# Performance work log

Measured on AMD Instinct MI355X. Metric: run time of the kernel, lower is better.

## Reference

```python
import jax, jax.numpy as jnp
import numpy as np

D_MODEL = 1024
N_HEADS = 16
HEAD_DIM = D_MODEL // N_HEADS
HIDDEN = 4096
EPS = 1e-5


def setup_inputs() -> dict:
    key = jax.random.key(0)
    ks = jax.random.split(key, 16)
    s = 1.0 / np.sqrt(D_MODEL)
    sh = 1.0 / np.sqrt(HIDDEN)
    inp = {
        'x': jax.random.normal(ks[0], (4, 2048, D_MODEL), dtype=jnp.float32),
        'Wq': jax.random.normal(ks[1], (D_MODEL, D_MODEL), dtype=jnp.float32) * s,
        'bq': jnp.zeros((D_MODEL,), jnp.float32),
        'Wk': jax.random.normal(ks[2], (D_MODEL, D_MODEL), dtype=jnp.float32) * s,
        'bk': jnp.zeros((D_MODEL,), jnp.float32),
        'Wv': jax.random.normal(ks[3], (D_MODEL, D_MODEL), dtype=jnp.float32) * s,
        'bv': jnp.zeros((D_MODEL,), jnp.float32),
        'Wo': jax.random.normal(ks[4], (D_MODEL, D_MODEL), dtype=jnp.float32) * s,
        'bo': jnp.zeros((D_MODEL,), jnp.float32),
        'gamma1': jnp.ones((D_MODEL,), jnp.float32),
        'beta1': jnp.zeros((D_MODEL,), jnp.float32),
        'W1': jax.random.normal(ks[5], (D_MODEL, HIDDEN), dtype=jnp.float32) * s,
        'b1': jnp.zeros((HIDDEN,), jnp.float32),
        'W2': jax.random.normal(ks[6], (HIDDEN, D_MODEL), dtype=jnp.float32) * sh,
        'b2': jnp.zeros((D_MODEL,), jnp.float32),
        'gamma2': jnp.ones((D_MODEL,), jnp.float32),
        'beta2': jnp.zeros((D_MODEL,), jnp.float32),
    }
    return inp


def _layernorm(x, gamma, beta):
    mu = jnp.mean(x, axis=-1, keepdims=True)
    var = jnp.mean(jnp.square(x - mu), axis=-1, keepdims=True)
    return (x - mu) * jax.lax.rsqrt(var + EPS) * gamma + beta


def _encoder_layer(x, Wq, bq, Wk, bk, Wv, bv, Wo, bo, gamma1, beta1,
                   W1, b1, W2, b2, gamma2, beta2):
    B, S, _ = x.shape
    # projections -> [B, H, S, Dh]
    def split_heads(t):
        return t.reshape(B, S, N_HEADS, HEAD_DIM).transpose(0, 2, 1, 3)
    q = split_heads(x @ Wq + bq)
    k = split_heads(x @ Wk + bk)
    v = split_heads(x @ Wv + bv)
    scale = 1.0 / jnp.sqrt(jnp.float32(HEAD_DIM))
    scores = jnp.einsum('bhqd,bhkd->bhqk', q, k) * scale
    attn = jax.nn.softmax(scores, axis=-1)
    ctx = jnp.einsum('bhqk,bhkd->bhqd', attn, v)
    ctx = ctx.transpose(0, 2, 1, 3).reshape(B, S, D_MODEL)
    attn_out = ctx @ Wo + bo
    # post-norm residual 1
    h = _layernorm(x + attn_out, gamma1, beta1)
    # MLP with exact (erf) GELU, as torch F.gelu default
    mlp = jax.nn.gelu(h @ W1 + b1, approximate=False) @ W2 + b2
    return _layernorm(h + mlp, gamma2, beta2)


def reference(x, Wq, bq, Wk, bk, Wv, bv, Wo, bo, gamma1, beta1,
              W1, b1, W2, b2, gamma2, beta2):
    return _encoder_layer(x, Wq, bq, Wk, bk, Wv, bv, Wo, bo, gamma1, beta1,
                          W1, b1, W2, b2, gamma2, beta2)
```

## Files before the change

kernel.cpp:

```cpp
#include <hip/hip_runtime.h>
#include <cstdint>
#include <cstddef>

using u16 = unsigned short;
using bf16x8 = __attribute__((ext_vector_type(8))) short;
using f32x4  = __attribute__((ext_vector_type(4))) float;

__device__ __forceinline__ u16 f2bf(float f) {
    union { float f; unsigned u; } v; v.f = f;
    unsigned r = v.u + 0x7fffu + ((v.u >> 16) & 1u);
    return (u16)(r >> 16);
}

__device__ __forceinline__ float bf2f(u16 b) {
    union { unsigned u; float f; } v; v.u = (unsigned)b << 16;
    return v.f;
}

__device__ __forceinline__ unsigned cvtpk(float lo, float hi) {
    unsigned r;
    asm("v_cvt_pk_bf16_f32 %0, %1, %2" : "=v"(r) : "v"(lo), "v"(hi));
    return r;
}

__device__ __forceinline__ float fexp2(float x) {
    float r;
    asm("v_exp_f32 %0, %1" : "=v"(r) : "v"(x));
    return r;
}

__device__ __forceinline__ float gelu_f(float x) {
    const float t2 = fminf(x * fmaf(0.10294825f, x * x, 2.3022082f), 80.f);
    const float e  = fexp2(t2);
    return x * e * __frcp_rn(e + 1.0f);
}

__device__ __forceinline__ void gld_lds16(const void* g, void* l) {
    __builtin_amdgcn_global_load_lds(
        (__attribute__((address_space(1))) void*)g,
        (__attribute__((address_space(3))) void*)l, 16, 0, 0);
}

__device__ __forceinline__ f32x4 mfma16(bf16x8 a, bf16x8 b, f32x4 c) {
    return __builtin_amdgcn_mfma_f32_16x16x32_bf16(a, b, c, 0, 0, 0);
}

__global__ __launch_bounds__(256)
void cast_kernel(const float* __restrict__ in, u16* __restrict__ out, int n8) {
    int i = blockIdx.x * 256 + threadIdx.x;
    if (i >= n8) return;
    const float4* p = (const float4*)in;
    float4 a = p[i * 2], b = p[i * 2 + 1];
    ushort4 r0 = make_ushort4(f2bf(a.x), f2bf(a.y), f2bf(a.z), f2bf(a.w));
    ushort4 r1 = make_ushort4(f2bf(b.x), f2bf(b.y), f2bf(b.z), f2bf(b.w));
    ((ushort4*)out)[i * 2]     = r0;
    ((ushort4*)out)[i * 2 + 1] = r1;
}

__global__ __launch_bounds__(256)
void tcast_all_kernel(const float* __restrict__ Wq, const float* __restrict__ Wk,
                      const float* __restrict__ Wv, const float* __restrict__ Wo,
                      const float* __restrict__ W1, const float* __restrict__ W2,
                      u16* __restrict__ wqkvt, u16* __restrict__ wot,
                      u16* __restrict__ w1t, u16* __restrict__ w2t)
{
    const int g = blockIdx.x;
    const float* src; u16* dst; int K, N, ti; float scale = 1.0f;
    if (g < 1024)      { src = Wq; dst = wqkvt;               K = 1024; N = 1024; ti = g;        scale = 0.18033688011112042f; }
    else if (g < 2048) { src = Wk; dst = wqkvt + 1048576;     K = 1024; N = 1024; ti = g - 1024; }
    else if (g < 3072) { src = Wv; dst = wqkvt + 2097152;     K = 1024; N = 1024; ti = g - 2048; }
    else if (g < 4096) { src = Wo; dst = wot;                 K = 1024; N = 1024; ti = g - 3072; }
    else if (g < 8192) { src = W1; dst = w1t;                 K = 1024; N = 4096; ti = g - 4096; }
    else               { src = W2; dst = w2t;                 K = 4096; N = 1024; ti = g - 8192; }
    const int nt = N >> 5;
    const int bx = ti % nt, by = ti / nt;
    const int k0 = by * 32, n0 = bx * 32;

    __shared__ float tile[32][33];
    const int tx = threadIdx.x & 31, ty = threadIdx.x >> 5;
    #pragma unroll
    for (int r = 0; r < 4; ++r) {
        int k = ty * 4 + r;
        tile[k][tx] = src[(size_t)(k0 + k) * N + n0 + tx];
    }
    __syncthreads();
    #pragma unroll
    for (int r = 0; r < 4; ++r) {
        int n = ty * 4 + r;
        dst[(size_t)(n0 + n) * K + k0 + tx] = f2bf(tile[tx][n] * scale);
    }
}

__global__ __launch_bounds__(256)
void bias_concat_kernel(const float* __restrict__ bq, const float* __restrict__ bk,
                        const float* __restrict__ bv, float* __restrict__ out) {
    int i = blockIdx.x * 256 + threadIdx.x;
    if (i >= 3072) return;
    float v;
    if (i < 1024)      v = bq[i] * 0.18033688011112042f;
    else if (i < 2048) v = bk[i - 1024];
    else               v = bv[i - 2048];
    out[i] = v;
}

template <int BM, int EPI>
__global__ __launch_bounds__(512, 1)
void gemm_pipe_kernel(const u16* __restrict__ A, const u16* __restrict__ Bt,
                      const float* __restrict__ bias, void* __restrict__ Cout,
                      int M, int N, int K)
{
    constexpr int AH  = BM * 64;
    constexpr int BH  = 16384;
    constexpr int BUF = 2 * AH + 2 * BH;
    constexpr int LPA = BM / 128;
    constexpr int VMN = LPA + 2;
    constexpr int MR  = BM / 32;
    constexpr int MRH = MR / 2;

    extern __shared__ char smem[];

    const int tid  = threadIdx.x;
    const int wid  = tid >> 6, lane = tid & 63;
    const int l15  = lane & 15, l4 = lane >> 4;
    const int wm   = wid >> 2, wn = wid & 3;

    const int nwg = gridDim.x;
    const int qx = nwg >> 3, rx = nwg & 7;
    const int orig = blockIdx.x;
    const int xcd = orig & 7, jx = orig >> 3;
    const int wgid = (xcd < rx ? xcd * (qx + 1) : rx * (qx + 1) + (xcd - rx) * qx) + jx;
    const int NTn = N / 256;
    const int m0 = (wgid / NTn) * BM;
    const int n0 = (wgid % NTn) * 256;

    const int q0 = tid >> 3, g0 = tid & 7;
    const int u0 = g0 ^ (q0 & 7);
    const int r0 = (q0 << 1) | (u0 >> 2), c80 = u0 & 3;
    const int q1 = q0 + 64;
    const int u1 = g0 ^ (q1 & 7);
    const int r1 = (q1 << 1) | (u1 >> 2), c81 = u1 & 3;
    const u16* aP0 = A  + (size_t)(m0 + r0) * K + c80 * 8;
    const u16* aP1 = A  + (size_t)(m0 + r1) * K + c81 * 8;
    const u16* bP0 = Bt + (size_t)(n0 + r0) * K + c80 * 8;
    const u16* bP1 = Bt + (size_t)(n0 + r1) * K + c81 * 8;
    const int NT = K >> 6;

    auto stageA = [&](int tt, int kk, int nb) {
        char* dst = smem + nb * BUF + kk * AH + tid * 16;
        const int kte = (tt << 6) + (kk << 5);
        gld_lds16(aP0 + kte, dst);
        if constexpr (LPA == 2) gld_lds16(aP1 + kte, dst + 8192);
    };
    auto stageB = [&](int tt, int kk, int nb) {
        char* dst = smem + nb * BUF + 2 * AH + kk * BH + tid * 16;
        const int kte = (tt << 6) + (kk << 5);
        gld_lds16(bP0 + kte, dst);
        gld_lds16(bP1 + kte, dst + 8192);
    };

    auto frag_off = [&](int row) -> int {
        const int q = row >> 1;
        const int u = ((row & 1) << 2) | l4;
        const int g = u ^ (q & 7);
        return q * 128 + g * 16;
    };

    f32x4 acc[MR][4];
    #pragma unroll
    for (int i = 0; i < MR; ++i)
        #pragma unroll
        for (int jj = 0; jj < 4; ++jj) acc[i][jj] = f32x4{0.f, 0.f, 0.f, 0.f};

    stageA(0, 0, 0); stageB(0, 0, 0); stageA(0, 1, 0); stageB(0, 1, 0);
    if constexpr (VMN == 4) asm volatile("s_waitcnt vmcnt(4)" ::: "memory");
    else                    asm volatile("s_waitcnt vmcnt(3)" ::: "memory");
    __builtin_amdgcn_s_barrier();
    asm volatile("" ::: "memory");

    for (int t = 0; t < NT; ++t) {
        const int cur = t & 1, nb = cur ^ 1;
        const int tn = (t + 1 < NT) ? t + 1 : t;
        const char* buf = smem + cur * BUF;
        bf16x8 bfr[4], af[MRH];

        #pragma unroll
        for (int kk = 0; kk < 2; ++kk) {
            #pragma unroll
            for (int fc = 0; fc < 4; ++fc)
                bfr[fc] = *(const bf16x8*)(buf + 2 * AH + kk * BH +
                                           frag_off(wn * 64 + fc * 16 + l15));
            #pragma unroll
            for (int i = 0; i < MRH; ++i)
                af[i] = *(const bf16x8*)(buf + kk * AH +
                                         frag_off(wm * (BM / 2) + i * 16 + l15));
            stageA(tn, kk, nb);
            asm volatile("" ::: "memory");
            __builtin_amdgcn_s_barrier();
            asm volatile("" ::: "memory");
            __builtin_amdgcn_s_setprio(1);
            #pragma unroll
            for (int i = 0; i < MRH; ++i)
                #pragma unroll
                for (int fc = 0; fc < 4; ++fc)
                    acc[i][fc] = mfma16(af[i], bfr[fc], acc[i][fc]);
            __builtin_amdgcn_s_setprio(0);

            #pragma unroll
            for (int i = 0; i < MRH; ++i)
                af[i] = *(const bf16x8*)(buf + kk * AH +
                                         frag_off(wm * (BM / 2) + (MRH + i) * 16 + l15));
            stageB(tn, kk, nb);
            if constexpr (VMN == 4) asm volatile("s_waitcnt vmcnt(4)" ::: "memory");
            else                    asm volatile("s_waitcnt vmcnt(3)" ::: "memory");
            __builtin_amdgcn_s_barrier();
            asm volatile("" ::: "memory");
            __builtin_amdgcn_s_setprio(1);
            #pragma unroll
            for (int i = 0; i < MRH; ++i)
                #pragma unroll
                for (int fc = 0; fc < 4; ++fc)
                    acc[MRH + i][fc] = mfma16(af[i], bfr[fc], acc[MRH + i][fc]);
            __builtin_amdgcn_s_setprio(0);
            asm volatile("" ::: "memory");
        }
    }

    float bv[4];
    #pragma unroll
    for (int fc = 0; fc < 4; ++fc) bv[fc] = bias[n0 + wn * 64 + fc * 16 + l15];
    #pragma unroll
    for (int fr = 0; fr < MR; ++fr) {
        const int rowg = m0 + wm * (BM / 2) + fr * 16 + l4 * 4;
        #pragma unroll
        for (int fc = 0; fc < 4; ++fc) {
            const int colg = n0 + wn * 64 + fc * 16 + l15;
            #pragma unroll
            for (int r = 0; r < 4; ++r) {
                const float v = acc[fr][fc][r] + bv[fc];
                const size_t off = (size_t)(rowg + r) * N + colg;
                if (EPI == 0) ((u16*)Cout)[off] = f2bf(v);
                else          ((u16*)Cout)[off] = f2bf(gelu_f(v));
            }
        }
    }
}

__global__ __launch_bounds__(256)
void vtrans_kernel(const u16* __restrict__ QKV, u16* __restrict__ Vt) {
    __shared__ u16 tile[64][68];
    const int t  = threadIdx.x;
    const int st = blockIdx.x, bh = blockIdx.y;
    const int b  = bh >> 4, h = bh & 15;
    #pragma unroll
    for (int i = 0; i < 2; ++i) {
        int sl = i * 32 + (t >> 3);
        const u16* gp = QKV + ((size_t)b * 2048 + st * 64 + sl) * 3072 + 2048 + h * 64 + (t & 7) * 8;
        ushort4 a = *(const ushort4*)gp;
        ushort4 c = *(const ushort4*)(gp + 4);
        u16* lp = &tile[sl][(t & 7) * 8];
        *(ushort4*)lp       = a;
        *(ushort4*)(lp + 4) = c;
    }
    __syncthreads();
    #pragma unroll
    for (int i = 0; i < 2; ++i) {
        int d  = i * 32 + (t >> 3);
        int s8 = (t & 7) * 8;
        ushort4 o0, o1;
        o0.x = tile[s8 + 0][d]; o0.y = tile[s8 + 1][d]; o0.z = tile[s8 + 2][d]; o0.w = tile[s8 + 3][d];
        o1.x = tile[s8 + 4][d]; o1.y = tile[s8 + 5][d]; o1.z = tile[s8 + 6][d]; o1.w = tile[s8 + 7][d];
        u16* op = Vt + ((size_t)bh * 64 + d) * 2048 + st * 64 + s8;
        *(ushort4*)op       = o0;
        *(ushort4*)(op + 4) = o1;
    }
}

__global__ __launch_bounds__(512)
void attn_kernel(const u16* __restrict__ QKV, const u16* __restrict__ Vt,
                 u16* __restrict__ ctx)
{
    __shared__ u16 smem[24576];

    const int tid = threadIdx.x;
    const int wid = tid >> 6, lane = tid & 63;
    const int l15 = lane & 15, l4 = lane >> 4;
    const int sw  = l15 & 7;
    const int lr  = lane >> 3;
    const int gsrc = ((lane & 7) ^ lr) * 8;
    const int g   = blockIdx.x;
    const int bh  = (g & 7) | ((g >> 6) << 3);
    const int qt  = (g >> 3) & 7;
    const int b = bh >> 4, h = bh & 15;
    const size_t qrow0 = (size_t)b * 2048 + (size_t)qt * 256;

    u16* const K0 = smem + 16384;
    u16* const V0 = smem + 20480;
    u16* const K1 = smem;
    u16* const V1 = smem + 4096;

    const u16* Qbase = QKV + h * 64;
    const u16* Kbase = QKV + (size_t)b * 2048 * 3072 + 1024 + h * 64;
    const u16* Vbase = Vt + (size_t)bh * 64 * 2048;

    #pragma unroll
    for (int c = 0; c < 4; ++c) {
        const int chunk = wid * 4 + c;
        const int row = chunk * 8 + lr;
        gld_lds16(Qbase + (qrow0 + row) * 3072 + gsrc,
                  (char*)smem + chunk * 1024);
    }

    auto stage_kv = [&](int kt, u16* kb, u16* vb) {
        const int rho = wid * 8 + lr;
        const int krow = (rho & 32) + ((rho & 16) >> 2) + ((rho & 12) << 1) + (rho & 3);
        gld_lds16(Kbase + (size_t)(kt + krow) * 3072 + gsrc,
                  (char*)kb + wid * 1024);
        gld_lds16(Vbase + (size_t)rho * 2048 + kt + gsrc,
                  (char*)vb + wid * 1024);
    };

    stage_kv(0, K0, V0);
    __syncthreads();

    bf16x8 qf[2][2];
    #pragma unroll
    for (int mi = 0; mi < 2; ++mi)
        #pragma unroll
        for (int kk = 0; kk < 2; ++kk)
            qf[mi][kk] = *(const bf16x8*)
                &smem[(size_t)(wid * 32 + mi * 16 + l15) * 64 + (((kk * 4 + l4) ^ sw) * 8)];
    __syncthreads();

    f32x4 accO[2][4] = {};
    f32x4 accL[2] = {};
    const short one_bf = (short)0x3F80;
    const bf16x8 ones = {one_bf, one_bf, one_bf, one_bf,
                         one_bf, one_bf, one_bf, one_bf};

    union U4 { unsigned u[4]; bf16x8 v; };

    auto compute_tile = [&](const u16* kb, const u16* vb) {
        f32x4 st[2][4];
        #pragma unroll
        for (int mi = 0; mi < 2; ++mi)
            #pragma unroll
            for (int ni = 0; ni < 4; ++ni) st[mi][ni] = f32x4{0.f, 0.f, 0.f, 0.f};
        __builtin_amdgcn_s_setprio(1);
        #pragma unroll
        for (int ni = 0; ni < 4; ++ni) {
            bf16x8 kf0 = *(const bf16x8*)&kb[(ni * 16 + l15) * 64 + ((l4 ^ sw) * 8)];
            bf16x8 kf1 = *(const bf16x8*)&kb[(ni * 16 + l15) * 64 + (((4 + l4) ^ sw) * 8)];
            #pragma unroll
            for (int mi = 0; mi < 2; ++mi) {
                st[mi][ni] = mfma16(kf0, qf[mi][0], st[mi][ni]);
                st[mi][ni] = mfma16(kf1, qf[mi][1], st[mi][ni]);
            }
        }
        __builtin_amdgcn_s_setprio(0);

        U4 pb[2][2];
        #pragma unroll
        for (int mi = 0; mi < 2; ++mi) {
            float p[4][4];
            #pragma unroll
            for (int ni = 0; ni < 4; ++ni)
                #pragma unroll
                for (int r = 0; r < 4; ++r)
                    p[ni][r] = fexp2(st[mi][ni][r]);
            #pragma unroll
            for (int ni = 0; ni < 4; ++ni) {
                pb[mi][ni >> 1].u[(ni & 1) * 2 + 0] = cvtpk(p[ni][0], p[ni][1]);
                pb[mi][ni >> 1].u[(ni & 1) * 2 + 1] = cvtpk(p[ni][2], p[ni][3]);
            }
        }

        __builtin_amdgcn_s_setprio(1);
        #pragma unroll
        for (int mi = 0; mi < 2; ++mi) {
            accL[mi] = mfma16(ones, pb[mi][0].v, accL[mi]);
            accL[mi] = mfma16(ones, pb[mi][1].v, accL[mi]);
        }
        #pragma unroll
        for (int di = 0; di < 4; ++di) {
            bf16x8 vf0 = *(const bf16x8*)&vb[(di * 16 + l15) * 64 + ((l4 ^ sw) * 8)];
            bf16x8 vf1 = *(const bf16x8*)&vb[(di * 16 + l15) * 64 + (((4 + l4) ^ sw) * 8)];
            #pragma unroll
            for (int mi = 0; mi < 2; ++mi) {
                accO[mi][di] = mfma16(vf0, pb[mi][0].v, accO[mi][di]);
                accO[mi][di] = mfma16(vf1, pb[mi][1].v, accO[mi][di]);
            }
        }
        __builtin_amdgcn_s_setprio(0);
    };

    for (int it = 0; it < 32; it += 2) {
        if (it + 1 < 32) stage_kv((it + 1) * 64, K1, V1);
        compute_tile(K0, V0);
        __syncthreads();
        if (it + 2 < 32) stage_kv((it + 2) * 64, K0, V0);
        compute_tile(K1, V1);
        __syncthreads();
    }

    #pragma unroll
    for (int mi = 0; mi < 2; ++mi) {
        const float inv = 1.0f / accL[mi][0];
        const size_t q = qrow0 + wid * 32 + mi * 16 + l15;
        #pragma unroll
        for (int di = 0; di < 4; ++di) {
            uint2 w;
            w.x = cvtpk(accO[mi][di][0] * inv, accO[mi][di][1] * inv);
            w.y = cvtpk(accO[mi][di][2] * inv, accO[mi][di][3] * inv);
            *(uint2*)&ctx[q * 1024 + h * 64 + di * 16 + l4 * 4] = w;
        }
    }
}

__global__ __launch_bounds__(256)
void add_ln_kernel(const u16* __restrict__ X, const u16* __restrict__ Y,
                   const float* __restrict__ gamma, const float* __restrict__ beta,
                   float* __restrict__ outf, u16* __restrict__ outb)
{
    const int row = blockIdx.x;
    const int t = threadIdx.x;
    const ushort4 xb = ((const ushort4*)(X + (size_t)row * 1024))[t];
    const ushort4 yb = ((const ushort4*)(Y + (size_t)row * 1024))[t];
    const float v0 = bf2f(xb.x) + bf2f(yb.x);
    const float v1 = bf2f(xb.y) + bf2f(yb.y);
    const float v2 = bf2f(xb.z) + bf2f(yb.z);
    const float v3 = bf2f(xb.w) + bf2f(yb.w);
    float s  = v0 + v1 + v2 + v3;
    float ss = v0 * v0 + v1 * v1 + v2 * v2 + v3 * v3;
    #pragma unroll
    for (int m = 1; m < 64; m <<= 1) {
        s  += __shfl_xor(s, m, 64);
        ss += __shfl_xor(ss, m, 64);
    }
    __shared__ float red[8];
    const int wid = t >> 6, lane = t & 63;
    if (lane == 0) { red[wid] = s; red[4 + wid] = ss; }
    __syncthreads();
    s  = red[0] + red[1] + red[2] + red[3];
    ss = red[4] + red[5] + red[6] + red[7];
    const float mu  = s * (1.f / 1024.f);
    const float var = ss * (1.f / 1024.f) - mu * mu;
    const float inv = rsqrtf(var + 1e-5f);
    const float4 g  = ((const float4*)gamma)[t];
    const float4 bb = ((const float4*)beta)[t];
    float4 o;
    o.x = (v0 - mu) * inv * g.x + bb.x;
    o.y = (v1 - mu) * inv * g.y + bb.y;
    o.z = (v2 - mu) * inv * g.z + bb.z;
    o.w = (v3 - mu) * inv * g.w + bb.w;
    if (outf != nullptr)
        ((float4*)(outf + (size_t)row * 1024))[t] = o;
    if (outb != nullptr) {
        ushort4 ob = make_ushort4(f2bf(o.x), f2bf(o.y), f2bf(o.z), f2bf(o.w));
        ((ushort4*)(outb + (size_t)row * 1024))[t] = ob;
    }
}

extern "C" void kernel_launch(void* const* d_in, const int* in_sizes, int n_in,
                              void* d_out, int out_size, void* d_ws, size_t ws_size,
                              hipStream_t stream)
{
    (void)in_sizes; (void)n_in; (void)out_size; (void)ws_size;
    const float* x   = (const float*)d_in[0];
    const float* Wq  = (const float*)d_in[1];
    const float* bq  = (const float*)d_in[2];
    const float* Wk  = (const float*)d_in[3];
    const float* bk  = (const float*)d_in[4];
    const float* Wv  = (const float*)d_in[5];
    const float* bv  = (const float*)d_in[6];
    const float* Wo  = (const float*)d_in[7];
    const float* bo  = (const float*)d_in[8];
    const float* g1  = (const float*)d_in[9];
    const float* be1 = (const float*)d_in[10];
    const float* W1  = (const float*)d_in[11];
    const float* b1  = (const float*)d_in[12];
    const float* W2  = (const float*)d_in[13];
    const float* b2  = (const float*)d_in[14];
    const float* g2  = (const float*)d_in[15];
    const float* be2 = (const float*)d_in[16];

    constexpr int M = 8192;
    constexpr int D = 1024;
    constexpr int F = 4096;

    char* ws = (char*)d_ws;
    size_t off = 0;
    auto nxt = [&](size_t bytes) -> char* {
        char* p = ws + off;
        off += (bytes + 255) & ~(size_t)255;
        return p;
    };
    u16*   xb    = (u16*)nxt((size_t)M * D * 2);
    u16*   wqkvt = (u16*)nxt((size_t)3 * D * D * 2);
    u16*   wot   = (u16*)nxt((size_t)D * D * 2);
    u16*   w1t   = (u16*)nxt((size_t)F * D * 2);
    u16*   w2t   = (u16*)nxt((size_t)D * F * 2);
    float* bqkv  = (float*)nxt(3072 * 4);
    u16*   qkv   = (u16*)nxt((size_t)M * 3 * D * 2);
    u16*   Vtb   = (u16*)nxt((size_t)M * D * 2);
    u16*   ctx   = (u16*)nxt((size_t)M * D * 2);
    u16*   attn  = (u16*)nxt((size_t)M * D * 2);
    u16*   hb    = (u16*)nxt((size_t)M * D * 2);
    u16*   t1    = qkv;
    u16*   mlp   = attn;

    cast_kernel<<<dim3(M * D / 8 / 256), dim3(256), 0, stream>>>(x, xb, M * D / 8);
    tcast_all_kernel<<<dim3(12288), dim3(256), 0, stream>>>(
        Wq, Wk, Wv, Wo, W1, W2, wqkvt, wot, w1t, w2t);
    bias_concat_kernel<<<dim3(12), dim3(256), 0, stream>>>(bq, bk, bv, bqkv);

    constexpr size_t LDS128 = 2 * (2 * 128 * 64 + 2 * 16384);
    constexpr size_t LDS256 = 2 * (2 * 256 * 64 + 2 * 16384);

    gemm_pipe_kernel<128, 0><<<dim3((M / 128) * (3 * D / 256)), dim3(512), LDS128, stream>>>(
        xb, wqkvt, bqkv, qkv, M, 3 * D, D);

    vtrans_kernel<<<dim3(2048 / 64, 64), dim3(256), 0, stream>>>(qkv, Vtb);
    attn_kernel<<<dim3(512), dim3(512), 0, stream>>>(qkv, Vtb, ctx);

    gemm_pipe_kernel<128, 0><<<dim3((M / 128) * (D / 256)), dim3(512), LDS128, stream>>>(
        ctx, wot, bo, attn, M, D, D);
    add_ln_kernel<<<dim3(M), dim3(256), 0, stream>>>(xb, attn, g1, be1, nullptr, hb);

    gemm_pipe_kernel<256, 2><<<dim3((M / 256) * (F / 256)), dim3(512), LDS256, stream>>>(
        hb, w1t, b1, t1, M, F, D);
    gemm_pipe_kernel<128, 0><<<dim3((M / 128) * (D / 256)), dim3(512), LDS128, stream>>>(
        t1, w2t, b2, mlp, M, D, F);
    add_ln_kernel<<<dim3(M), dim3(256), 0, stream>>>(hb, mlp, g2, be2, (float*)d_out, nullptr);
}
```

Before: 359.6 us.

## Split attention key tiles across wave pairs and reduce partial outputs in LDS

```diff
diff --git a/kernel.cpp b/kernel.cpp
--- a/kernel.cpp
+++ b/kernel.cpp
@@ -194,6 +194,7 @@
                 af[i] = *(const bf16x8*)(buf + kk * AH +
                                          frag_off(wm * (BM / 2) + i * 16 + l15));
             stageA(tn, kk, nb);
+            stageB(tn, kk, nb);
             asm volatile("" ::: "memory");
             __builtin_amdgcn_s_barrier();
             asm volatile("" ::: "memory");
@@ -209,7 +210,6 @@
             for (int i = 0; i < MRH; ++i)
                 af[i] = *(const bf16x8*)(buf + kk * AH +
                                          frag_off(wm * (BM / 2) + (MRH + i) * 16 + l15));
-            stageB(tn, kk, nb);
             if constexpr (VMN == 4) asm volatile("s_waitcnt vmcnt(4)" ::: "memory");
             else                    asm volatile("s_waitcnt vmcnt(3)" ::: "memory");
             __builtin_amdgcn_s_barrier();
@@ -292,6 +292,7 @@
     const int qt  = (g >> 3) & 7;
     const int b = bh >> 4, h = bh & 15;
     const size_t qrow0 = (size_t)b * 2048 + (size_t)qt * 256;
+    const int qg = wid & 3, kh = wid >> 2;
 
     u16* const K0 = smem + 16384;
     u16* const V0 = smem + 20480;
@@ -322,17 +323,17 @@
     stage_kv(0, K0, V0);
     __syncthreads();
 
-    bf16x8 qf[2][2];
-    #pragma unroll
-    for (int mi = 0; mi < 2; ++mi)
-        #pragma unroll
-        for (int kk = 0; kk < 2; ++kk)
-            qf[mi][kk] = *(const bf16x8*)
-                &smem[(size_t)(wid * 32 + mi * 16 + l15) * 64 + (((kk * 4 + l4) ^ sw) * 8)];
-    __syncthreads();
-
-    f32x4 accO[2][4] = {};
-    f32x4 accL[2] = {};
+    bf16x8 qf[4][2];
+    #pragma unroll
+    for (int mi = 0; mi < 4; ++mi)
+        #pragma unroll
+        for (int kkq = 0; kkq < 2; ++kkq)
+            qf[mi][kkq] = *(const bf16x8*)
+                &smem[(size_t)(qg * 64 + mi * 16 + l15) * 64 + (((kkq * 4 + l4) ^ sw) * 8)];
+    __syncthreads();
+
+    f32x4 accO[4][4] = {};
+    float accL[4] = {};
     const short one_bf = (short)0x3F80;
     const bf16x8 ones = {one_bf, one_bf, one_bf, one_bf,
                          one_bf, one_bf, one_bf, one_bf};
@@ -340,55 +341,52 @@
     union U4 { unsigned u[4]; bf16x8 v; };
 
     auto compute_tile = [&](const u16* kb, const u16* vb) {
-        f32x4 st[2][4];
-        #pragma unroll
-        for (int mi = 0; mi < 2; ++mi)
-            #pragma unroll
-            for (int ni = 0; ni < 4; ++ni) st[mi][ni] = f32x4{0.f, 0.f, 0.f, 0.f};
+        f32x4 st[4][2];
+        #pragma unroll
+        for (int mi = 0; mi < 4; ++mi)
+            #pragma unroll
+            for (int nl = 0; nl < 2; ++nl) st[mi][nl] = f32x4{0.f, 0.f, 0.f, 0.f};
         __builtin_amdgcn_s_setprio(1);
         #pragma unroll
-        for (int ni = 0; ni < 4; ++ni) {
+        for (int nl = 0; nl < 2; ++nl) {
+            const int ni = kh * 2 + nl;
             bf16x8 kf0 = *(const bf16x8*)&kb[(ni * 16 + l15) * 64 + ((l4 ^ sw) * 8)];
             bf16x8 kf1 = *(const bf16x8*)&kb[(ni * 16 + l15) * 64 + (((4 + l4) ^ sw) * 8)];
             #pragma unroll
-            for (int mi = 0; mi < 2; ++mi) {
-                st[mi][ni] = mfma16(kf0, qf[mi][0], st[mi][ni]);
-                st[mi][ni] = mfma16(kf1, qf[mi][1], st[mi][ni]);
+            for (int mi = 0; mi < 4; ++mi) {
+                st[mi][nl] = mfma16(kf0, qf[mi][0], st[mi][nl]);
+                st[mi][nl] = mfma16(kf1, qf[mi][1], st[mi][nl]);
             }
         }
         __builtin_amdgcn_s_setprio(0);
 
-        U4 pb[2][2];
-        #pragma unroll
-        for (int mi = 0; mi < 2; ++mi) {
-            float p[4][4];
-            #pragma unroll
-            for (int ni = 0; ni < 4; ++ni)
+        U4 pb[4];
+        #pragma unroll
+        for (int mi = 0; mi < 4; ++mi) {
+            float p[2][4];
+            #pragma unroll
+            for (int nl = 0; nl < 2; ++nl)
                 #pragma unroll
                 for (int r = 0; r < 4; ++r)
-                    p[ni][r] = fexp2(st[mi][ni][r]);
-            #pragma unroll
-            for (int ni = 0; ni < 4; ++ni) {
-                pb[mi][ni >> 1].u[(ni & 1) * 2 + 0] = cvtpk(p[ni][0], p[ni][1]);
-                pb[mi][ni >> 1].u[(ni & 1) * 2 + 1] = cvtpk(p[ni][2], p[ni][3]);
-            }
+                    p[nl][r] = fexp2(st[mi][nl][r]);
+            pb[mi].u[0] = cvtpk(p[0][0], p[0][1]);
+            pb[mi].u[1] = cvtpk(p[0][2], p[0][3]);
+            pb[mi].u[2] = cvtpk(p[1][0], p[1][1]);
+            pb[mi].u[3] = cvtpk(p[1][2], p[1][3]);
         }
 
         __builtin_amdgcn_s_setprio(1);
         #pragma unroll
-        for (int mi = 0; mi < 2; ++mi) {
-            accL[mi] = mfma16(ones, pb[mi][0].v, accL[mi]);
-            accL[mi] = mfma16(ones, pb[mi][1].v, accL[mi]);
+        for (int mi = 0; mi < 4; ++mi) {
+            f32x4 lz = mfma16(ones, pb[mi].v, f32x4{0.f, 0.f, 0.f, 0.f});
+            accL[mi] += lz[0];
         }
         #pragma unroll
         for (int di = 0; di < 4; ++di) {
-            bf16x8 vf0 = *(const bf16x8*)&vb[(di * 16 + l15) * 64 + ((l4 ^ sw) * 8)];
-            bf16x8 vf1 = *(const bf16x8*)&vb[(di * 16 + l15) * 64 + (((4 + l4) ^ sw) * 8)];
-            #pragma unroll
-            for (int mi = 0; mi < 2; ++mi) {
-                accO[mi][di] = mfma16(vf0, pb[mi][0].v, accO[mi][di]);
-                accO[mi][di] = mfma16(vf1, pb[mi][1].v, accO[mi][di]);
-            }
+            bf16x8 vf = *(const bf16x8*)&vb[(di * 16 + l15) * 64 + (((kh * 4 + l4) ^ sw) * 8)];
+            #pragma unroll
+            for (int mi = 0; mi < 4; ++mi)
+                accO[mi][di] = mfma16(vf, pb[mi].v, accO[mi][di]);
         }
         __builtin_amdgcn_s_setprio(0);
     };
@@ -402,16 +400,62 @@
         __syncthreads();
     }
 
-    #pragma unroll
-    for (int mi = 0; mi < 2; ++mi) {
-        const float inv = 1.0f / accL[mi][0];
-        const size_t q = qrow0 + wid * 32 + mi * 16 + l15;
-        #pragma unroll
-        for (int di = 0; di < 4; ++di) {
-            uint2 w;
-            w.x = cvtpk(accO[mi][di][0] * inv, accO[mi][di][1] * inv);
-            w.y = cvtpk(accO[mi][di][2] * inv, accO[mi][di][3] * inv);
-            *(uint2*)&ctx[q * 1024 + h * 64 + di * 16 + l4 * 4] = w;
+    float* red = (float*)smem;
+    __syncthreads();
+    if (kh == 1) {
+        #pragma unroll
+        for (int mi = 0; mi < 2; ++mi)
+            #pragma unroll
+            for (int di = 0; di < 4; ++di)
+                *(f32x4*)&red[(((qg * 2 + mi) * 4 + di) * 64 + lane) * 4] = accO[mi][di];
+        #pragma unroll
+        for (int mi = 0; mi < 4; ++mi)
+            red[8192 + (qg * 4 + mi) * 64 + lane] = accL[mi];
+    }
+    __syncthreads();
+    if (kh == 0) {
+        #pragma unroll
+        for (int mi = 0; mi < 2; ++mi)
+            #pragma unroll
+            for (int di = 0; di < 4; ++di) {
+                f32x4 o = *(const f32x4*)&red[(((qg * 2 + mi) * 4 + di) * 64 + lane) * 4];
+                accO[mi][di][0] += o[0]; accO[mi][di][1] += o[1];
+                accO[mi][di][2] += o[2]; accO[mi][di][3] += o[3];
+            }
+        #pragma unroll
+        for (int mi = 0; mi < 4; ++mi)
+            accL[mi] += red[8192 + (qg * 4 + mi) * 64 + lane];
+    }
+    __syncthreads();
+    if (kh == 1) {
+        #pragma unroll
+        for (int mi = 2; mi < 4; ++mi)
+            #pragma unroll
+            for (int di = 0; di < 4; ++di)
+                *(f32x4*)&red[(((qg * 2 + (mi - 2)) * 4 + di) * 64 + lane) * 4] = accO[mi][di];
+    }
+    __syncthreads();
+    if (kh == 0) {
+        #pragma unroll
+        for (int mi = 2; mi < 4; ++mi)
+            #pragma unroll
+            for (int di = 0; di < 4; ++di) {
+                f32x4 o = *(const f32x4*)&red[(((qg * 2 + (mi - 2)) * 4 + di) * 64 + lane) * 4];
+                accO[mi][di][0] += o[0]; accO[mi][di][1] += o[1];
+                accO[mi][di][2] += o[2]; accO[mi][di][3] += o[3];
+            }
+
+        #pragma unroll
+        for (int mi = 0; mi < 4; ++mi) {
+            const float inv = 1.0f / accL[mi];
+            const size_t q = qrow0 + qg * 64 + mi * 16 + l15;
+            #pragma unroll
+            for (int di = 0; di < 4; ++di) {
+                uint2 w;
+                w.x = cvtpk(accO[mi][di][0] * inv, accO[mi][di][1] * inv);
+                w.y = cvtpk(accO[mi][di][2] * inv, accO[mi][di][3] * inv);
+                *(uint2*)&ctx[q * 1024 + h * 64 + di * 16 + l4 * 4] = w;
+            }
         }
     }
 }
```

After: 366.1 us. About the same (+1.8%).

## Deepen GEMM prefetch to three half-tiles ahead with one barrier per k-half

Applied to the files above, without the earlier changes.

```diff
diff --git a/kernel.cpp b/kernel.cpp
--- a/kernel.cpp
+++ b/kernel.cpp
@@ -84,10 +84,14 @@
         tile[k][tx] = src[(size_t)(k0 + k) * N + n0 + tx];
     }
     __syncthreads();
-    #pragma unroll
-    for (int r = 0; r < 4; ++r) {
-        int n = ty * 4 + r;
-        dst[(size_t)(n0 + n) * K + k0 + tx] = f2bf(tile[tx][n] * scale);
+    const int kx = (threadIdx.x & 15) * 2;
+    const int ny = threadIdx.x >> 4;
+    #pragma unroll
+    for (int r = 0; r < 2; ++r) {
+        const int n = ny * 2 + r;
+        ushort2 o = make_ushort2(f2bf(tile[kx][n] * scale),
+                                 f2bf(tile[kx + 1][n] * scale));
+        *(ushort2*)&dst[(size_t)(n0 + n) * K + k0 + kx] = o;
     }
 }
 
@@ -113,9 +117,8 @@
     constexpr int BH  = 16384;
     constexpr int BUF = 2 * AH + 2 * BH;
     constexpr int LPA = BM / 128;
-    constexpr int VMN = LPA + 2;
+    constexpr int GRP = LPA + 2;
     constexpr int MR  = BM / 32;
-    constexpr int MRH = MR / 2;
 
     extern __shared__ char smem[];
 
@@ -144,18 +147,16 @@
     const u16* bP0 = Bt + (size_t)(n0 + r0) * K + c80 * 8;
     const u16* bP1 = Bt + (size_t)(n0 + r1) * K + c81 * 8;
     const int NT = K >> 6;
-
-    auto stageA = [&](int tt, int kk, int nb) {
-        char* dst = smem + nb * BUF + kk * AH + tid * 16;
+    const int NTm1 = NT - 1;
+
+    auto stageAB = [&](int tt, int kk, int sb) {
         const int kte = (tt << 6) + (kk << 5);
-        gld_lds16(aP0 + kte, dst);
-        if constexpr (LPA == 2) gld_lds16(aP1 + kte, dst + 8192);
-    };
-    auto stageB = [&](int tt, int kk, int nb) {
-        char* dst = smem + nb * BUF + 2 * AH + kk * BH + tid * 16;
-        const int kte = (tt << 6) + (kk << 5);
-        gld_lds16(bP0 + kte, dst);
-        gld_lds16(bP1 + kte, dst + 8192);
+        char* da = smem + sb * BUF + kk * AH + tid * 16;
+        gld_lds16(aP0 + kte, da);
+        if constexpr (LPA == 2) gld_lds16(aP1 + kte, da + 8192);
+        char* db = smem + sb * BUF + 2 * AH + kk * BH + tid * 16;
+        gld_lds16(bP0 + kte, db);
+        gld_lds16(bP1 + kte, db + 8192);
     };
 
     auto frag_off = [&](int row) -> int {
@@ -171,17 +172,15 @@
         #pragma unroll
         for (int jj = 0; jj < 4; ++jj) acc[i][jj] = f32x4{0.f, 0.f, 0.f, 0.f};
 
-    stageA(0, 0, 0); stageB(0, 0, 0); stageA(0, 1, 0); stageB(0, 1, 0);
-    if constexpr (VMN == 4) asm volatile("s_waitcnt vmcnt(4)" ::: "memory");
-    else                    asm volatile("s_waitcnt vmcnt(3)" ::: "memory");
+    stageAB(0, 0, 0); stageAB(0, 1, 0); stageAB(1, 0, 1);
+    if constexpr (GRP == 4) asm volatile("s_waitcnt vmcnt(8)" ::: "memory");
+    else                    asm volatile("s_waitcnt vmcnt(6)" ::: "memory");
     __builtin_amdgcn_s_barrier();
     asm volatile("" ::: "memory");
 
     for (int t = 0; t < NT; ++t) {
-        const int cur = t & 1, nb = cur ^ 1;
-        const int tn = (t + 1 < NT) ? t + 1 : t;
-        const char* buf = smem + cur * BUF;
-        bf16x8 bfr[4], af[MRH];
+        const char* buf = smem + (t & 1) * BUF;
+        bf16x8 bfr[4], af[MR];
 
         #pragma unroll
         for (int kk = 0; kk < 2; ++kk) {
@@ -190,36 +189,26 @@
                 bfr[fc] = *(const bf16x8*)(buf + 2 * AH + kk * BH +
                                            frag_off(wn * 64 + fc * 16 + l15));
             #pragma unroll
-            for (int i = 0; i < MRH; ++i)
+            for (int i = 0; i < MR; ++i)
                 af[i] = *(const bf16x8*)(buf + kk * AH +
                                          frag_off(wm * (BM / 2) + i * 16 + l15));
-            stageA(tn, kk, nb);
-            asm volatile("" ::: "memory");
+            if (kk == 0) {
+                const int tt = (t + 1 <= NTm1) ? t + 1 : NTm1;
+                stageAB(tt, 1, (t + 1) & 1);
+            } else {
+                const int tt = (t + 2 <= NTm1) ? t + 2 : NTm1;
+                stageAB(tt, 0, t & 1);
+            }
+            if constexpr (GRP == 4) asm volatile("s_waitcnt vmcnt(8)" ::: "memory");
+            else                    asm volatile("s_waitcnt vmcnt(6)" ::: "memory");
             __builtin_amdgcn_s_barrier();
             asm volatile("" ::: "memory");
             __builtin_amdgcn_s_setprio(1);
             #pragma unroll
-            for (int i = 0; i < MRH; ++i)
+            for (int i = 0; i < MR; ++i)
                 #pragma unroll
                 for (int fc = 0; fc < 4; ++fc)
                     acc[i][fc] = mfma16(af[i], bfr[fc], acc[i][fc]);
-            __builtin_amdgcn_s_setprio(0);
-
-            #pragma unroll
-            for (int i = 0; i < MRH; ++i)
-                af[i] = *(const bf16x8*)(buf + kk * AH +
-                                         frag_off(wm * (BM / 2) + (MRH + i) * 16 + l15));
-            stageB(tn, kk, nb);
-            if constexpr (VMN == 4) asm volatile("s_waitcnt vmcnt(4)" ::: "memory");
-            else                    asm volatile("s_waitcnt vmcnt(3)" ::: "memory");
-            __builtin_amdgcn_s_barrier();
-            asm volatile("" ::: "memory");
-            __builtin_amdgcn_s_setprio(1);
-            #pragma unroll
-            for (int i = 0; i < MRH; ++i)
-                #pragma unroll
-                for (int fc = 0; fc < 4; ++fc)
-                    acc[MRH + i][fc] = mfma16(af[i], bfr[fc], acc[MRH + i][fc]);
             __builtin_amdgcn_s_setprio(0);
             asm volatile("" ::: "memory");
         }
```

Result: no change. 356.6 us (-0.8%).
